# Optimization experiments

Hardware: AMD Instinct MI355X
Metric: run time of the kernel (lower is better)

Reference implementation:

```python
import jax, jax.numpy as jnp
import numpy as np


def setup_inputs() -> dict:
    key = jax.random.key(0)
    ks = jax.random.split(key, 7)
    B, C, W, H = 4, 128, 64, 64
    Cq = C // 8
    x = jax.random.normal(ks[0], (B, C, W, H), jnp.float32)
    wq = jax.random.normal(ks[1], (Cq, C), jnp.float32) * 0.05
    bq = jax.random.normal(ks[2], (Cq,), jnp.float32) * 0.05
    wk = jax.random.normal(ks[3], (Cq, C), jnp.float32) * 0.05
    bk = jax.random.normal(ks[4], (Cq,), jnp.float32) * 0.05
    wv = jax.random.normal(ks[5], (C, C), jnp.float32) * 0.05
    bv = jax.random.normal(ks[6], (C,), jnp.float32) * 0.05
    gamma = jnp.ones((1,), jnp.float32)
    return {"x": x, "wq": wq, "bq": bq, "wk": wk, "bk": bk,
            "wv": wv, "bv": bv, "gamma": gamma}


def reference(x, wq, bq, wk, bk, wv, bv, gamma):
    B, C, W, H = x.shape
    N = W * H
    xf = x.reshape(B, C, N)  # flatten spatial dims (W fastest over H, as torch .view)
    # 1x1 convs == per-position linear maps
    q = jnp.einsum('dc,bcn->bnd', wq, xf) + bq            # [B, N, C//8]
    k = jnp.einsum('dc,bcn->bdn', wk, xf) + bk[:, None]   # [B, C//8, N]
    v = jnp.einsum('dc,bcn->bdn', wv, xf) + bv[:, None]   # [B, C, N]
    energy = jnp.einsum('bnd,bdm->bnm', q, k)             # [B, N, N]
    # block-causal mask: position i may attend only to j < (i//W + 1)*W
    i = jnp.arange(N)
    j = jnp.arange(N)
    masked = j[None, :] >= ((i[:, None] // W) + 1) * W    # True -> -inf
    energy = jnp.where(masked[None, :, :], -jnp.inf, energy)
    attention = jax.nn.softmax(energy, axis=-1)           # [B, N, N]
    # out[b,c,n] = sum_m V[b,c,m] * attn[b,n,m]  (torch bmm(V, attn^T))
    out = jnp.einsum('bcm,bnm->bcn', v, attention).reshape(B, C, W, H)
    out = gamma * out + x
    return (out, attention)
```

## Files before the change

### kernel.cpp

```cpp
#include <hip/hip_runtime.h>
#include <hip/hip_bf16.h>


typedef __attribute__((ext_vector_type(8))) short short8;
typedef __attribute__((ext_vector_type(16))) float float16;

__device__ __forceinline__ ushort f2bf(float f) {
  union { float f; uint u; } v; v.f = f;
  return (ushort)((v.u + 0x7FFFu + ((v.u >> 16) & 1u)) >> 16);
}

#define LDS_BARRIER()                                             \
  do {                                                            \
    __builtin_amdgcn_sched_barrier(0);                            \
    asm volatile("s_waitcnt lgkmcnt(0)" ::: "memory");            \
    __builtin_amdgcn_sched_barrier(0);                            \
    __builtin_amdgcn_s_barrier();                                 \
    __builtin_amdgcn_sched_barrier(0);                            \
  } while (0)

__global__ __launch_bounds__(512, 2) void qkv_kernel(
    const float* __restrict__ x,
    const float* __restrict__ wq, const float* __restrict__ bq,
    const float* __restrict__ wk, const float* __restrict__ bk,
    const float* __restrict__ wv, const float* __restrict__ bv,
    ushort* __restrict__ qT, ushort* __restrict__ kT, ushort* __restrict__ vo) {
  __shared__ float xs[128 * 64];
  const int nt = blockIdx.x, b = blockIdx.y;
  const int n0 = nt * 64;
  const float* xb = x + (size_t)b * 524288 + n0;
  for (int idx = threadIdx.x; idx < 8192; idx += 512) {
    int c = idx >> 6, n = idx & 63;
    xs[idx] = xb[(size_t)c * 4096 + n];
  }
  __syncthreads();
  const int n = threadIdx.x & 63;
  const int og = __builtin_amdgcn_readfirstlane((int)(threadIdx.x >> 6));
  float acc[20];
#pragma unroll
  for (int i = 0; i < 20; i++) {
    int o = og + 8 * i;
    acc[i] = (i < 2) ? bq[o] : (i < 4) ? bk[o - 16] : bv[o - 32];
  }
#pragma unroll 4
  for (int c = 0; c < 128; c++) {
    float xr = xs[c * 64 + n];
#pragma unroll
    for (int i = 0; i < 20; i++) {
      int o = og + 8 * i;
      const float* wr = (i < 2) ? (wq + o * 128)
                      : (i < 4) ? (wk + (o - 16) * 128)
                                : (wv + (o - 32) * 128);
      acc[i] += wr[c] * xr;
    }
  }
  const size_t pos = (size_t)b * 4096 + n0 + n;
#pragma unroll
  for (int i = 0; i < 20; i++) {
    int o = og + 8 * i;
    if (i < 2)      qT[pos * 16 + o]      = f2bf(acc[i]);
    else if (i < 4) kT[pos * 16 + o - 16] = f2bf(acc[i]);
    else vo[(size_t)b * 524288 + (size_t)(o - 32) * 4096 + n0 + n] = f2bf(acc[i]);
  }
}

__global__ __launch_bounds__(256, 2) void fused_attn_kernel(
    const ushort* __restrict__ qT, const ushort* __restrict__ kT,
    const ushort* __restrict__ vws, const float* __restrict__ x,
    const float* __restrict__ g,
    float* __restrict__ attn, float* __restrict__ out) {
  __shared__ __align__(16) ushort Pt[4][32 * 72];
  __shared__ __align__(16) float red[32][4];
  const int bx = blockIdx.x;
  const int b = bx & 3;
  const int v_ = bx >> 2;
  const int half = v_ & 1;
  const int u = v_ >> 1;
  const int rb = (u < 32) ? u : 95 - u;
  const int S = rb + 1;
  const int lane = threadIdx.x & 63;
  const int w = __builtin_amdgcn_readfirstlane((int)(threadIdx.x >> 6));
  const int nblk = rb * 64 + half * 32;
  const int l31 = lane & 31;
  const int h = lane >> 5;
  const int hk = h * 8;
  const ushort* qb = qT + (size_t)b * 65536;
  const ushort* kb = kT + (size_t)b * 65536;
  const ushort* vp = vws + (size_t)b * 524288;
  float* ab = attn + (size_t)b * 16777216;

  const short8 qa = *(const short8*)(qb + (size_t)(nblk + l31) * 16 + hk);

  float16 zero16;
#pragma unroll
  for (int i = 0; i < 16; i++) zero16[i] = 0.f;

  float sume[16];
#pragma unroll
  for (int i = 0; i < 16; i++) sume[i] = 0.f;
  for (int s = w; s < S; s += 4) {
    const int m0 = s * 64;
#pragma unroll
    for (int mh = 0; mh < 2; mh++) {
      short8 kf = *(const short8*)(kb + (size_t)(m0 + mh * 32 + l31) * 16 + hk);
      float16 e = __builtin_amdgcn_mfma_f32_32x32x16_bf16(qa, kf, zero16, 0, 0, 0);
#pragma unroll
      for (int r = 0; r < 16; r++) sume[r] += __expf(e[r]);
    }
  }
#pragma unroll
  for (int r = 0; r < 16; r++) {
#pragma unroll
    for (int off = 1; off <= 16; off <<= 1)
      sume[r] += __shfl_xor(sume[r], off, 64);
  }
  if (l31 == 0) {
#pragma unroll
    for (int r = 0; r < 16; r++) {
      int row = (r & 3) + 8 * (r >> 2) + 4 * h;
      red[row][w] = sume[r];
    }
  }
  __syncthreads();
  float inv[16];
#pragma unroll
  for (int r = 0; r < 16; r++) {
    int row = (r & 3) + 8 * (r >> 2) + 4 * h;
    float4 p4 = *(const float4*)&red[row][0];
    inv[r] = 1.0f / (p4.x + p4.y + p4.z + p4.w);
  }

  float16 acc = zero16;
  for (int s0 = 0; s0 < S; s0 += 4) {
    const int sl = (S - s0 < 4) ? (S - s0) : 4;
    if (w < sl) {
      const int m0 = (s0 + w) * 64;
      ushort* Pb = &Pt[w][0];
#pragma unroll
      for (int mh = 0; mh < 2; mh++) {
        short8 kf = *(const short8*)(kb + (size_t)(m0 + mh * 32 + l31) * 16 + hk);
        float16 e = __builtin_amdgcn_mfma_f32_32x32x16_bf16(qa, kf, zero16, 0, 0, 0);
#pragma unroll
        for (int r = 0; r < 16; r++) {
          int row = (r & 3) + 8 * (r >> 2) + 4 * h;
          float p = __expf(e[r]) * inv[r];
          ab[(size_t)(nblk + row) * 4096 + m0 + mh * 32 + l31] = p;
          Pb[row * 72 + mh * 32 + l31] = f2bf(p);
        }
      }
    }
    LDS_BARRIER();
    for (int ss = 0; ss < sl; ss++) {
      const int m0 = (s0 + ss) * 64;
      const ushort* vrow = vp + (size_t)(w * 32 + l31) * 4096 + m0 + hk;
      const ushort* Pr = &Pt[ss][l31 * 72 + hk];
#pragma unroll
      for (int kk = 0; kk < 4; kk++) {
        short8 a  = *(const short8*)(vrow + kk * 16);
        short8 bf = *(const short8*)(Pr + kk * 16);
        acc = __builtin_amdgcn_mfma_f32_32x32x16_bf16(a, bf, acc, 0, 0, 0);
      }
    }
    LDS_BARRIER();
  }

  const int M = S * 64;
  const int Z4 = (4096 - M) >> 2;
  const float4 z = make_float4(0.f, 0.f, 0.f, 0.f);
#pragma unroll
  for (int r = 0; r < 8; r++) {
    float4* dst = (float4*)(ab + (size_t)(nblk + w * 8 + r) * 4096 + M);
    for (int i4 = lane; i4 < Z4; i4 += 64) dst[i4] = z;
  }

  const float gamma = g[0];
#pragma unroll
  for (int reg = 0; reg < 16; reg++) {
    int row = (reg & 3) + 8 * (reg >> 2) + 4 * h;
    int c = w * 32 + row;
    int n = nblk + l31;
    size_t off = (size_t)b * 524288 + (size_t)c * 4096 + n;
    out[off] = gamma * acc[reg] + x[off];
  }
}

extern "C" void kernel_launch(void* const* d_in, const int* in_sizes, int n_in,
                              void* d_out, int out_size, void* d_ws, size_t ws_size,
                              hipStream_t stream) {
  const float* x  = (const float*)d_in[0];
  const float* wq = (const float*)d_in[1];
  const float* bq = (const float*)d_in[2];
  const float* wk = (const float*)d_in[3];
  const float* bk = (const float*)d_in[4];
  const float* wv = (const float*)d_in[5];
  const float* bv = (const float*)d_in[6];
  const float* gm = (const float*)d_in[7];
  float* out  = (float*)d_out;
  float* attn = out + 2097152;
  ushort* qTw = (ushort*)d_ws;
  ushort* kTw = qTw + 262144;
  ushort* vws = qTw + 524288;

  qkv_kernel<<<dim3(64, 4), 512, 0, stream>>>(x, wq, bq, wk, bk, wv, bv, qTw, kTw, vws);
  fused_attn_kernel<<<dim3(512), 256, 0, stream>>>(qTw, kTw, vws, x, gm, attn, out);
}
```

Baseline: 353.1 us.

## Double attention block to 8 waves with split-K PV and LDS reduction

The fused attention block grows from 4 to 8 waves. The row-sum pass and the probability-tile pass now cover 8 column tiles per step. The PV accumulation is split over two wave halves by key tile, and the two partial accumulators are combined through shared memory before the output is written. The aim is more parallelism per block, so the exp and attention-write phase is less serialized and more latency is hidden. In exchange it adds an extra LDS reduction and barrier, doubles the LDS tile buffer, and puts more register pressure on the tighter launch bounds.

```diff
diff --git a/kernel.cpp b/kernel.cpp
--- a/kernel.cpp
+++ b/kernel.cpp
@@ -4,6 +4,7 @@
 
 typedef __attribute__((ext_vector_type(8))) short short8;
 typedef __attribute__((ext_vector_type(16))) float float16;
+typedef __attribute__((ext_vector_type(4))) float floatx4;
 
 __device__ __forceinline__ ushort f2bf(float f) {
   union { float f; uint u; } v; v.f = f;
@@ -64,13 +65,13 @@
   }
 }
 
-__global__ __launch_bounds__(256, 2) void fused_attn_kernel(
+__global__ __launch_bounds__(512, 4) void fused_attn_kernel(
     const ushort* __restrict__ qT, const ushort* __restrict__ kT,
     const ushort* __restrict__ vws, const float* __restrict__ x,
     const float* __restrict__ g,
     float* __restrict__ attn, float* __restrict__ out) {
-  __shared__ __align__(16) ushort Pt[4][32 * 72];
-  __shared__ __align__(16) float red[32][4];
+  __shared__ __align__(16) ushort Pt[8][32 * 72];
+  __shared__ __align__(16) float red[32][8];
   const int bx = blockIdx.x;
   const int b = bx & 3;
   const int v_ = bx >> 2;
@@ -80,6 +81,8 @@
   const int S = rb + 1;
   const int lane = threadIdx.x & 63;
   const int w = __builtin_amdgcn_readfirstlane((int)(threadIdx.x >> 6));
+  const int q = w & 3;
+  const int hh = w >> 2;
   const int nblk = rb * 64 + half * 32;
   const int l31 = lane & 31;
   const int h = lane >> 5;
@@ -98,7 +101,7 @@
   float sume[16];
 #pragma unroll
   for (int i = 0; i < 16; i++) sume[i] = 0.f;
-  for (int s = w; s < S; s += 4) {
+  for (int s = w; s < S; s += 8) {
     const int m0 = s * 64;
 #pragma unroll
     for (int mh = 0; mh < 2; mh++) {
@@ -126,13 +129,15 @@
 #pragma unroll
   for (int r = 0; r < 16; r++) {
     int row = (r & 3) + 8 * (r >> 2) + 4 * h;
-    float4 p4 = *(const float4*)&red[row][0];
-    inv[r] = 1.0f / (p4.x + p4.y + p4.z + p4.w);
+    const float* pr = &red[row][0];
+    float t = ((pr[0] + pr[1]) + (pr[2] + pr[3])) +
+              ((pr[4] + pr[5]) + (pr[6] + pr[7]));
+    inv[r] = 1.0f / t;
   }
 
   float16 acc = zero16;
-  for (int s0 = 0; s0 < S; s0 += 4) {
-    const int sl = (S - s0 < 4) ? (S - s0) : 4;
+  for (int s0 = 0; s0 < S; s0 += 8) {
+    const int sl = (S - s0 < 8) ? (S - s0) : 8;
     if (w < sl) {
       const int m0 = (s0 + w) * 64;
       ushort* Pb = &Pt[w][0];
@@ -150,9 +155,9 @@
       }
     }
     LDS_BARRIER();
-    for (int ss = 0; ss < sl; ss++) {
+    for (int ss = hh; ss < sl; ss += 2) {
       const int m0 = (s0 + ss) * 64;
-      const ushort* vrow = vp + (size_t)(w * 32 + l31) * 4096 + m0 + hk;
+      const ushort* vrow = vp + (size_t)(q * 32 + l31) * 4096 + m0 + hk;
       const ushort* Pr = &Pt[ss][l31 * 72 + hk];
 #pragma unroll
       for (int kk = 0; kk < 4; kk++) {
@@ -164,23 +169,38 @@
     LDS_BARRIER();
   }
 
+  float* accx = (float*)&Pt[0][0];
+  if (hh == 1) {
+#pragma unroll
+    for (int reg = 0; reg < 16; reg++)
+      accx[reg * 256 + q * 64 + lane] = acc[reg];
+  }
+  __syncthreads();
+  if (hh == 0) {
+#pragma unroll
+    for (int reg = 0; reg < 16; reg++)
+      acc[reg] += accx[reg * 256 + q * 64 + lane];
+  }
+
   const int M = S * 64;
   const int Z4 = (4096 - M) >> 2;
-  const float4 z = make_float4(0.f, 0.f, 0.f, 0.f);
-#pragma unroll
-  for (int r = 0; r < 8; r++) {
-    float4* dst = (float4*)(ab + (size_t)(nblk + w * 8 + r) * 4096 + M);
+  const floatx4 z = {0.f, 0.f, 0.f, 0.f};
+#pragma unroll
+  for (int r = 0; r < 4; r++) {
+    floatx4* dst = (floatx4*)(ab + (size_t)(nblk + w * 4 + r) * 4096 + M);
     for (int i4 = lane; i4 < Z4; i4 += 64) dst[i4] = z;
   }
 
-  const float gamma = g[0];
-#pragma unroll
-  for (int reg = 0; reg < 16; reg++) {
-    int row = (reg & 3) + 8 * (reg >> 2) + 4 * h;
-    int c = w * 32 + row;
-    int n = nblk + l31;
-    size_t off = (size_t)b * 524288 + (size_t)c * 4096 + n;
-    out[off] = gamma * acc[reg] + x[off];
+  if (hh == 0) {
+    const float gamma = g[0];
+#pragma unroll
+    for (int reg = 0; reg < 16; reg++) {
+      int row = (reg & 3) + 8 * (reg >> 2) + 4 * h;
+      int c = q * 32 + row;
+      int n = nblk + l31;
+      size_t off = (size_t)b * 524288 + (size_t)c * 4096 + n;
+      out[off] = gamma * acc[reg] + x[off];
+    }
   }
 }
 
@@ -202,5 +222,5 @@
   ushort* vws = qTw + 524288;
 
   qkv_kernel<<<dim3(64, 4), 512, 0, stream>>>(x, wq, bq, wk, bk, wv, bv, qTw, kTw, vws);
-  fused_attn_kernel<<<dim3(512), 256, 0, stream>>>(qTw, kTw, vws, x, gm, attn, out);
-}
+  fused_attn_kernel<<<dim3(512), 512, 0, stream>>>(qTw, kTw, vws, x, gm, attn, out);
+}
```

After: 347.5 us. No clear change (-1.6%).
